# Kernel tuning notes

Measured on AMD Instinct MI355X. Metric: run time of the kernel, lower is better.

## Reference

```python
import jax, jax.numpy as jnp
import numpy as np

B, L, H, NH = 4, 2048, 1024, 8
DK = H // NH   # head_k_dim = 128
DV = H // NH   # head_v_dim = 128
CONV_K, FIR_S, FIR_L = 4, 3, 31
CMAX = 0.2
EPS = 1e-5
CHUNK = 32


def _l2norm(x):
    return x * jax.lax.rsqrt(jnp.sum(x * x, -1, keepdims=True) + 1e-6)


def _rms(x, w):
    return x * jax.lax.rsqrt(jnp.mean(x * x, -1, keepdims=True) + EPS) * w


def _causal_conv(x, w):
    # x: [b, l, d], w: [d, K] depthwise causal FIR (ShortConvolution)
    K = w.shape[1]
    l = x.shape[1]
    xp = jnp.pad(x, ((0, 0), (K - 1, 0), (0, 0)))
    return sum(xp[:, i:i + l, :] * w[:, i][None, None, :] for i in range(K))


def _fir(x, w):
    # x: [b, l, h, d], w: [h, d, K] per-head depthwise causal FIR
    K = w.shape[-1]
    l = x.shape[1]
    xp = jnp.pad(x, ((0, 0), (K - 1, 0), (0, 0), (0, 0)))
    return sum(xp[:, i:i + l] * w[:, :, i][None, None] for i in range(K))


def _delta_rule_chunkwise(q, k, v, beta, chunk=CHUNK):
    # q,k: [b,h,L,dk]; v: [b,h,L,dv]; beta: [b,h,L]; L % chunk == 0
    b, h, Ln, dk = q.shape
    dv = v.shape[-1]
    n = Ln // chunk
    q = _l2norm(q)
    k = _l2norm(k)
    v = v * beta[..., None]
    kb = k * beta[..., None]
    rs = lambda t: t.reshape(b, h, n, chunk, t.shape[-1])
    qc, kc, vc, kbc = rs(q), rs(k), rs(v), rs(kb)
    mask_incl = jnp.triu(jnp.ones((chunk, chunk), dtype=bool), 0)
    mask_strict = jnp.triu(jnp.ones((chunk, chunk), dtype=bool), 1)
    # UT / WY transform: sequential Gaussian-elimination over chunk rows
    attn = jnp.where(mask_incl, 0.0, -(kbc @ jnp.swapaxes(kc, -1, -2)))
    for i in range(1, chunk):
        row = attn[..., i, :]                                   # [b,h,n,c]
        upd = jnp.einsum('bhnj,bhnjk->bhnk', row, attn[..., :i])  # [b,h,n,i]
        attn = attn.at[..., i, :i].add(upd)
    attn = attn + jnp.eye(chunk, dtype=attn.dtype)
    u = attn @ vc    # [b,h,n,c,dv]
    w = attn @ kbc   # [b,h,n,c,dk]
    # sequential scan over chunks carrying state S [b,h,dk,dv]
    mv = lambda t: jnp.moveaxis(t, 2, 0)  # [n,b,h,c,d]
    def step(S, xs):
        q_i, k_i, u_i, w_i = xs
        attn_local = jnp.where(mask_strict, 0.0, q_i @ jnp.swapaxes(k_i, -1, -2))
        u_new = u_i - w_i @ S
        o_i = q_i @ S + attn_local @ u_new
        S = S + jnp.swapaxes(k_i, -1, -2) @ u_new
        return S, o_i
    S0 = jnp.zeros((b, h, dk, dv), dtype=q.dtype)
    S, o = jax.lax.scan(step, S0, (mv(qc), mv(kc), mv(u), mv(w)))
    o = jnp.moveaxis(o, 0, 2).reshape(b, h, Ln, dv)
    return o, S


def _forward(hidden_states, Wq, Wk, Wv, Wb, conv_q_w, conv_k_w, conv_v_w,
             fir_short_w, fir_long_w, floor_W, floor_b, fus_W1, fus_b1,
             fus_W2, fus_b2, norm_pf_w, norm_o_w, Wo):
    b, l, _ = hidden_states.shape
    hs = hidden_states
    q_lin = jax.nn.silu(_causal_conv(hs @ Wq, conv_q_w))
    k_lin = jax.nn.silu(_causal_conv(hs @ Wk, conv_k_w))
    v_lin = jax.nn.silu(_causal_conv(hs @ Wv, conv_v_w))
    q = q_lin.reshape(b, l, NH, DK)
    k = k_lin.reshape(b, l, NH, DK)
    v_direct = v_lin.reshape(b, l, NH, DV)
    beta = jax.nn.sigmoid(hs @ Wb)  # [b,l,h]
    delta_out_t, _ = _delta_rule_chunkwise(
        jnp.transpose(q, (0, 2, 1, 3)), jnp.transpose(k, (0, 2, 1, 3)),
        jnp.transpose(v_direct, (0, 2, 1, 3)), jnp.transpose(beta, (0, 2, 1)))
    delta_out = jnp.transpose(delta_out_t, (0, 2, 1, 3))  # [b,l,h,dv]
    local_short = _fir(v_direct, fir_short_w)
    local_long = _fir(v_direct, fir_long_w)
    floor = jax.nn.sigmoid(hs @ floor_W + floor_b) * CMAX  # [b,l,h]
    fus = jax.nn.gelu(hs @ fus_W1 + fus_b1, approximate=False) @ fus_W2 + fus_b2
    fus = fus.reshape(b, l, NH, 4)
    p_value = jax.nn.sigmoid(fus[..., 3]) * (1.0 - floor)  # context share >= floor
    ctx = jax.nn.softmax(fus[..., :3], axis=-1) * (1.0 - p_value)[..., None]
    o = (ctx[..., 0, None] * local_short + ctx[..., 1, None] * local_long
         + ctx[..., 2, None] * delta_out + p_value[..., None] * v_direct)
    o = _rms(o, norm_pf_w)
    o = _rms(o, norm_o_w)
    return o.reshape(b, l, NH * DV) @ Wo


def setup_inputs() -> dict:
    key = jax.random.key(0)
    ks = jax.random.split(key, 16)
    n = lambda k, shape, s=0.02: jax.random.normal(k, shape, jnp.float32) * s
    fus_b2 = jnp.zeros((NH * 4,), jnp.float32).at[3::4].set(4.0)
    return {
        'hidden_states': jax.random.normal(ks[0], (B, L, H), jnp.float32),
        'Wq': n(ks[1], (H, H)), 'Wk': n(ks[2], (H, H)), 'Wv': n(ks[3], (H, H)),
        'Wb': n(ks[4], (H, NH)),
        'conv_q_w': n(ks[5], (H, CONV_K), 0.2),
        'conv_k_w': n(ks[6], (H, CONV_K), 0.2),
        'conv_v_w': n(ks[7], (H, CONV_K), 0.2),
        'fir_short_w': n(ks[8], (NH, DV, FIR_S), 0.2),
        'fir_long_w': n(ks[9], (NH, DV, FIR_L), 0.2),
        'floor_W': n(ks[10], (H, NH)),
        'floor_b': jnp.full((NH,), float(np.log(CMAX / (1 - CMAX))), jnp.float32),
        'fus_W1': n(ks[11], (H, 2 * H)), 'fus_b1': jnp.zeros((2 * H,), jnp.float32),
        'fus_W2': n(ks[12], (2 * H, NH * 4)), 'fus_b2': fus_b2,
        'norm_pf_w': jnp.ones((DV,), jnp.float32),
        'norm_o_w': jnp.ones((DV,), jnp.float32),
        'Wo': n(ks[13], (H, H)),
    }


def reference(hidden_states, Wq, Wk, Wv, Wb, conv_q_w, conv_k_w, conv_v_w,
              fir_short_w, fir_long_w, floor_W, floor_b, fus_W1, fus_b1,
              fus_W2, fus_b2, norm_pf_w, norm_o_w, Wo):
    return _forward(hidden_states, Wq, Wk, Wv, Wb, conv_q_w, conv_k_w, conv_v_w,
                    fir_short_w, fir_long_w, floor_W, floor_b, fus_W1, fus_b1,
                    fus_W2, fus_b2, norm_pf_w, norm_o_w, Wo)
```

## Files before the change

kernel.cpp:

```cpp
#include <hip/hip_runtime.h>
#include <hip/hip_bf16.h>
#include <cstdint>
#include <cstddef>

#define DEVI static __device__ __forceinline__

typedef __attribute__((ext_vector_type(4))) float f32x4;
typedef __attribute__((ext_vector_type(8))) short s16x8;
typedef unsigned short u16;
typedef unsigned int u32;

DEVI float bf2f(u16 u){ u32 x = ((u32)u) << 16; float f; __builtin_memcpy(&f, &x, 4); return f; }
DEVI u16 f2bf(float f){ u32 x; __builtin_memcpy(&x, &f, 4); u32 r = x + 0x7fffu + ((x >> 16) & 1u); return (u16)(r >> 16); }
DEVI float sigm(float x){ return 1.0f / (1.0f + expf(-x)); }
DEVI f32x4 mfma16(s16x8 a, s16x8 b, f32x4 c){ return __builtin_amdgcn_mfma_f32_16x16x32_bf16(a, b, c, 0, 0, 0); }
DEVI s16x8 pack8(float4 a, float4 b){
  s16x8 v;
  v[0]=(short)f2bf(a.x); v[1]=(short)f2bf(a.y); v[2]=(short)f2bf(a.z); v[3]=(short)f2bf(a.w);
  v[4]=(short)f2bf(b.x); v[5]=(short)f2bf(b.y); v[6]=(short)f2bf(b.z); v[7]=(short)f2bf(b.w);
  return v;
}
DEVI u32 pkbf(float lo, float hi){
  u32 d; asm("v_cvt_pk_bf16_f32 %0, %1, %2" : "=v"(d) : "v"(lo), "v"(hi));
  return d;
}
DEVI s16x8 ld_tr(const u16* p){
  short4 a = *(const short4*)p;
  short4 b = *(const short4*)(p + 4);
  s16x8 v; v[0]=a.x; v[1]=a.y; v[2]=a.z; v[3]=a.w; v[4]=b.x; v[5]=b.y; v[6]=b.z; v[7]=b.w;
  return v;
}

#define GLL16(gp, lp) __builtin_amdgcn_global_load_lds( \
    (const __attribute__((address_space(1))) void*)(gp), \
    (__attribute__((address_space(3))) void*)(lp), 16, 0, 0)

__global__ __launch_bounds__(256) void cvt_bf16_k(const float* __restrict__ src, u16* __restrict__ dst, int n4){
  int i = blockIdx.x * 256 + threadIdx.x;
  if (i < n4){
    float4 v = ((const float4*)src)[i];
    ushort4 o; o.x = f2bf(v.x); o.y = f2bf(v.y); o.z = f2bf(v.z); o.w = f2bf(v.w);
    ((ushort4*)dst)[i] = o;
  }
}

__global__ __launch_bounds__(256) void transpose_bf16_k(const float* __restrict__ src, u16* __restrict__ dst, int K, int N){
  __shared__ float tile[32][33];
  const int n0 = blockIdx.x * 32, k0 = blockIdx.y * 32;
  const int t = threadIdx.x, cc = t & 31, rb = t >> 5;
  #pragma unroll
  for (int it = 0; it < 4; ++it){ int rr = rb + it*8; tile[rr][cc] = src[(size_t)(k0+rr)*N + n0 + cc]; }
  __syncthreads();
  #pragma unroll
  for (int it = 0; it < 4; ++it){ int rr = rb + it*8; dst[(size_t)(n0+rr)*K + k0 + cc] = f2bf(tile[cc][rr]); }
}

__global__ __launch_bounds__(64) void w2pack_k(const float* __restrict__ W2, u16* __restrict__ w2p){
  const int kt = blockIdx.x, nt = blockIdx.y;
  const int lane = threadIdx.x, g = lane >> 4, r = lane & 15;
  float v[8];
  #pragma unroll
  for (int i=0;i<8;++i) v[i] = W2[(size_t)(kt*32 + g*8 + i)*32 + nt*16 + r];
  *(s16x8*)(w2p + (((size_t)kt*2 + nt)*64 + lane)*8) = pack8(make_float4(v[0],v[1],v[2],v[3]),
                                                             make_float4(v[4],v[5],v[6],v[7]));
}

__global__ __launch_bounds__(64) void wbpack_k(const float* __restrict__ Wb, const float* __restrict__ Wfl,
                                              u16* __restrict__ wbp){
  const int kt = blockIdx.x;
  const int lane = threadIdx.x, g = lane >> 4, r = lane & 15;
  float v[8];
  #pragma unroll
  for (int i=0;i<8;++i){
    const int k = kt*32 + g*8 + i;
    v[i] = (r < 8) ? Wb[(size_t)k*8 + r] : Wfl[(size_t)k*8 + (r-8)];
  }
  *(s16x8*)(wbp + ((size_t)kt*64 + lane)*8) = pack8(make_float4(v[0],v[1],v[2],v[3]),
                                                    make_float4(v[4],v[5],v[6],v[7]));
}

template<int EPI>
__global__ __launch_bounds__(256, 2) void gemm_bt(
    const u16* __restrict__ A, const u16* __restrict__ Bt, void* __restrict__ Cout,
    const float* __restrict__ bias, int M, int N, int K)
{
  __shared__ __align__(16) u16 As[128*64];
  __shared__ __align__(16) u16 Bs[128*64];
  const int t = threadIdx.x;
  const int lane = t & 63, w = t >> 6;
  const int wr = w >> 1, wc = w & 1;
  const int g = lane >> 4, r16 = lane & 15;
  const int nwg = gridDim.x * gridDim.y;
  const int bid = blockIdx.x + blockIdx.y * gridDim.x;
  const int swz = (bid & 7) * (nwg >> 3) + (bid >> 3);
  const int m0 = (swz / gridDim.x) * 128, n0 = (swz % gridDim.x) * 128;
  f32x4 acc[4][4];
  #pragma unroll
  for (int i=0;i<4;++i){ f32x4 z = {0,0,0,0}; acc[i][0]=z; acc[i][1]=z; acc[i][2]=z; acc[i][3]=z; }
  const int NK = K / 64;
  const int slot_l = w*64 + lane;
  for (int kt = 0; kt < NK; ++kt){
    __syncthreads();
    #pragma unroll
    for (int j=0;j<4;++j){
      const int sl = j*256 + slot_l;
      const int row = sl >> 3, ch = sl & 7;
      const int chs = ch ^ (row & 7);
      GLL16(A  + (size_t)(m0+row)*K + kt*64 + chs*8, As + (size_t)(j*256 + w*64)*8);
      GLL16(Bt + (size_t)(n0+row)*K + kt*64 + chs*8, Bs + (size_t)(j*256 + w*64)*8);
    }
    __syncthreads();
    #pragma unroll
    for (int kh = 0; kh < 2; ++kh){
      s16x8 af[4], bf_[4];
      #pragma unroll
      for (int i=0;i<4;++i){
        const int arow = wr*64 + i*16 + r16;
        af[i]  = *(const s16x8*)(As + (size_t)arow*64 + (((4*kh+g) ^ (arow&7)))*8);
        const int brow = wc*64 + i*16 + r16;
        bf_[i] = *(const s16x8*)(Bs + (size_t)brow*64 + (((4*kh+g) ^ (brow&7)))*8);
      }
      #pragma unroll
      for (int mi=0;mi<4;++mi)
        #pragma unroll
        for (int ni=0;ni<4;++ni)
          acc[mi][ni] = mfma16(af[mi], bf_[ni], acc[mi][ni]);
    }
  }
  #pragma unroll
  for (int mi=0;mi<4;++mi)
    #pragma unroll
    for (int ni=0;ni<4;++ni){
      const int col = n0 + wc*64 + ni*16 + r16;
      #pragma unroll
      for (int i=0;i<4;++i){
        const int row = m0 + wr*64 + mi*16 + g*4 + i;
        float v = acc[mi][ni][i];
        if (EPI == 0){
          ((u16*)Cout)[(size_t)row*N + col] = f2bf(v);
        } else if (EPI == 1){
          float x = v + bias[col];
          x = 0.5f * x * (1.0f + erff(x * 0.70710678118f));
          ((u16*)Cout)[(size_t)row*N + col] = f2bf(x);
        } else if (EPI == 2){
          ((float*)Cout)[(size_t)row*N + col] = v;
        } else {
          ((u16*)Cout)[(size_t)(col >> 10)*8388608 + (size_t)row*1024 + (col & 1023)] = f2bf(v);
        }
      }
    }
}

__global__ __launch_bounds__(64) void beta_floor_k(
    const u16* __restrict__ hsb, const u16* __restrict__ wbp, const float* __restrict__ flb,
    float* __restrict__ beta, float* __restrict__ flo)
{
  const int m0 = blockIdx.x * 16;
  const int lane = threadIdx.x, g = lane >> 4, r = lane & 15;
  f32x4 acc0 = {0,0,0,0}, acc1 = {0,0,0,0};
  #pragma unroll 4
  for (int kt = 0; kt < 32; kt += 2){
    s16x8 a0 = *(const s16x8*)(hsb + (size_t)(m0+r)*1024 + kt*32 + g*8);
    s16x8 b0 = *(const s16x8*)(wbp + ((size_t)kt*64 + lane)*8);
    s16x8 a1 = *(const s16x8*)(hsb + (size_t)(m0+r)*1024 + (kt+1)*32 + g*8);
    s16x8 b1 = *(const s16x8*)(wbp + ((size_t)(kt+1)*64 + lane)*8);
    acc0 = mfma16(a0, b0, acc0);
    acc1 = mfma16(a1, b1, acc1);
  }
  const float fb = (r >= 8) ? flb[r-8] : 0.f;
  #pragma unroll
  for (int i=0;i<4;++i){
    const int row = m0 + g*4 + i;
    const float v = acc0[i] + acc1[i];
    if (r < 8) beta[(size_t)row*8 + r] = sigm(v);
    else       flo [(size_t)row*8 + (r-8)] = 0.2f * sigm(v + fb);
  }
}

__global__ __launch_bounds__(256) void conv_silu_k(
    const u16* __restrict__ qraw, const u16* __restrict__ kraw, const u16* __restrict__ vraw,
    const float* __restrict__ cwq, const float* __restrict__ cwk, const float* __restrict__ cwv,
    u16* __restrict__ vdir, u16* __restrict__ qn, u16* __restrict__ kn)
{
  const int blk = blockIdx.x;
  const int b = blk >> 7, lt = blk & 127;
  const int l0 = lt * 16;
  const int t = threadIdx.x, c0 = t * 4;
  float wq[16], wk[16], wv[16];
  #pragma unroll
  for (int cc=0; cc<4; ++cc){
    float4 a = *(const float4*)(cwq + (size_t)(c0+cc)*4);
    wq[cc*4+0]=a.x; wq[cc*4+1]=a.y; wq[cc*4+2]=a.z; wq[cc*4+3]=a.w;
    float4 bq = *(const float4*)(cwk + (size_t)(c0+cc)*4);
    wk[cc*4+0]=bq.x; wk[cc*4+1]=bq.y; wk[cc*4+2]=bq.z; wk[cc*4+3]=bq.w;
    float4 c = *(const float4*)(cwv + (size_t)(c0+cc)*4);
    wv[cc*4+0]=c.x; wv[cc*4+1]=c.y; wv[cc*4+2]=c.z; wv[cc*4+3]=c.w;
  }
  float hq[3][4], hk[3][4], hv[3][4];
  #pragma unroll
  for (int i=0;i<3;++i){
    const int ls = l0 - 3 + i;
    if (ls >= 0){
      const size_t base = ((size_t)(b << 11) + ls)*1024 + c0;
      union{ ushort4 v; u16 s[4]; } xq, xk, xv;
      xq.v = *(const ushort4*)(qraw + base);
      xk.v = *(const ushort4*)(kraw + base);
      xv.v = *(const ushort4*)(vraw + base);
      #pragma unroll
      for (int cc=0;cc<4;++cc){ hq[i][cc]=bf2f(xq.s[cc]); hk[i][cc]=bf2f(xk.s[cc]); hv[i][cc]=bf2f(xv.s[cc]); }
    } else {
      #pragma unroll
      for (int cc=0;cc<4;++cc){ hq[i][cc]=0.f; hk[i][cc]=0.f; hv[i][cc]=0.f; }
    }
  }
  float cq[4], ck4[4], cv4[4], nq[4], nk[4], nv[4];
  {
    const size_t base = ((size_t)(b << 11) + l0)*1024 + c0;
    union{ ushort4 v; u16 s[4]; } xq, xk, xv;
    xq.v = *(const ushort4*)(qraw + base);
    xk.v = *(const ushort4*)(kraw + base);
    xv.v = *(const ushort4*)(vraw + base);
    #pragma unroll
    for (int cc=0;cc<4;++cc){ cq[cc]=bf2f(xq.s[cc]); ck4[cc]=bf2f(xk.s[cc]); cv4[cc]=bf2f(xv.s[cc]); }
  }
  const int head = c0 >> 7, d0 = c0 & 127;
  for (int rr = 0; rr < 16; ++rr){
    const int l = l0 + rr;
    if (rr < 15){
      const size_t base = ((size_t)(b << 11) + l + 1)*1024 + c0;
      union{ ushort4 v; u16 s[4]; } xq, xk, xv;
      xq.v = *(const ushort4*)(qraw + base);
      xk.v = *(const ushort4*)(kraw + base);
      xv.v = *(const ushort4*)(vraw + base);
      #pragma unroll
      for (int cc=0;cc<4;++cc){ nq[cc]=bf2f(xq.s[cc]); nk[cc]=bf2f(xk.s[cc]); nv[cc]=bf2f(xv.s[cc]); }
    }
    float qa[4], ka[4], va[4];
    #pragma unroll
    for (int cc=0; cc<4; ++cc){
      qa[cc] = hq[0][cc]*wq[cc*4+0] + hq[1][cc]*wq[cc*4+1] + hq[2][cc]*wq[cc*4+2] + cq[cc]*wq[cc*4+3];
      ka[cc] = hk[0][cc]*wk[cc*4+0] + hk[1][cc]*wk[cc*4+1] + hk[2][cc]*wk[cc*4+2] + ck4[cc]*wk[cc*4+3];
      va[cc] = hv[0][cc]*wv[cc*4+0] + hv[1][cc]*wv[cc*4+1] + hv[2][cc]*wv[cc*4+2] + cv4[cc]*wv[cc*4+3];
    }
    #pragma unroll
    for (int cc=0; cc<4; ++cc){
      qa[cc] = qa[cc]*sigm(qa[cc]); ka[cc] = ka[cc]*sigm(ka[cc]); va[cc] = va[cc]*sigm(va[cc]);
    }
    const int grow = (b << 11) + l;
    ushort4 ov; ov.x=f2bf(va[0]); ov.y=f2bf(va[1]); ov.z=f2bf(va[2]); ov.w=f2bf(va[3]);
    *(ushort4*)(vdir + (size_t)grow*1024 + c0) = ov;
    float ssq = 0.f, ssk = 0.f;
    #pragma unroll
    for (int cc=0; cc<4; ++cc){ ssq += qa[cc]*qa[cc]; ssk += ka[cc]*ka[cc]; }
    #pragma unroll
    for (int m=1; m<32; m<<=1){ ssq += __shfl_xor(ssq, m, 64); ssk += __shfl_xor(ssk, m, 64); }
    const float rq = rsqrtf(ssq + 1e-6f), rk = rsqrtf(ssk + 1e-6f);
    const size_t ob = (((size_t)(b*8 + head))*2048 + l)*128 + d0;
    ushort4 oq, ok;
    oq.x=f2bf(qa[0]*rq); oq.y=f2bf(qa[1]*rq); oq.z=f2bf(qa[2]*rq); oq.w=f2bf(qa[3]*rq);
    ok.x=f2bf(ka[0]*rk); ok.y=f2bf(ka[1]*rk); ok.z=f2bf(ka[2]*rk); ok.w=f2bf(ka[3]*rk);
    *(ushort4*)(qn + ob) = oq;
    *(ushort4*)(kn + ob) = ok;
    #pragma unroll
    for (int cc=0; cc<4; ++cc){
      hq[0][cc]=hq[1][cc]; hq[1][cc]=hq[2][cc]; hq[2][cc]=cq[cc];  cq[cc]=nq[cc];
      hk[0][cc]=hk[1][cc]; hk[1][cc]=hk[2][cc]; hk[2][cc]=ck4[cc]; ck4[cc]=nk[cc];
      hv[0][cc]=hv[1][cc]; hv[1][cc]=hv[2][cc]; hv[2][cc]=cv4[cc]; cv4[cc]=nv[cc];
    }
  }
}

__global__ __launch_bounds__(64) void fus2_k(
    const u16* __restrict__ A, const u16* __restrict__ w2p, const float* __restrict__ b2,
    float* __restrict__ out)
{
  const int m0 = blockIdx.x * 16;
  const int lane = threadIdx.x, g = lane >> 4, r = lane & 15;
  f32x4 acc[2][2];
  #pragma unroll
  for (int nt=0;nt<2;++nt){ f32x4 z = {0,0,0,0}; acc[nt][0]=z; acc[nt][1]=z; }
  #pragma unroll 4
  for (int kt = 0; kt < 64; ++kt){
    s16x8 af = *(const s16x8*)(A + (size_t)(m0+r)*2048 + kt*32 + g*8);
    s16x8 b0 = *(const s16x8*)(w2p + (((size_t)kt*2 + 0)*64 + lane)*8);
    s16x8 b1 = *(const s16x8*)(w2p + (((size_t)kt*2 + 1)*64 + lane)*8);
    acc[0][kt&1] = mfma16(af, b0, acc[0][kt&1]);
    acc[1][kt&1] = mfma16(af, b1, acc[1][kt&1]);
  }
  #pragma unroll
  for (int nt=0;nt<2;++nt){
    const float bb = b2[nt*16 + r];
    #pragma unroll
    for (int i=0;i<4;++i)
      out[(size_t)(m0 + g*4 + i)*32 + nt*16 + r] = acc[nt][0][i] + acc[nt][1][i] + bb;
  }
}

__global__ __launch_bounds__(256, 2) void ut_k(
    const u16* __restrict__ qn, const u16* __restrict__ kn,
    const u16* __restrict__ vdir, const float* __restrict__ beta,
    u16* __restrict__ alocp, u16* __restrict__ updk,
    u16* __restrict__ wpk, u16* __restrict__ knpk)
{
  __shared__ __align__(16) char smem[39680];
  u16*  k_s = (u16*)smem;
  float* Tm = (float*)smem;
  float* Gm = (float*)(smem + 8192);
  float* al = (float*)(smem + 12416);
  float* wl = (float*)(smem + 8192);
  u16*  knT = (u16*)(smem + 17024);
  u16*  vbT = (u16*)(smem + 28288);
  float* bet = (float*)(smem + 39552);

  const int blk = blockIdx.x;
  const int ic = blk & 63, bh = blk >> 6;
  const int b = bh >> 3, h = bh & 7;
  const int l0 = ic * 32;
  const int t = threadIdx.x;
  const int lane = t & 63, w = t >> 6;
  const int g = lane >> 4, r = lane & 15;
  const int mt = w >> 1, nt_g = w & 1;

  const size_t gqk = ((size_t)bh*2048 + l0)*128;

  {
    const int row = t >> 3, sseg = t & 7;
    #pragma unroll
    for (int ss=0; ss<2; ++ss){
      const int s = sseg + ss*8;
      int4 kv = *(const int4*)(kn + gqk + (size_t)row*128 + s*8);
      *(int4*)((char*)k_s + row*256 + ((s ^ (row&7))*16)) = kv;
    }
  }
  {
    const int rp = t & 15, cs = t >> 4;
    const int r0 = 2*rp, r1 = 2*rp + 1;
    union { s16x8 v; u16 u[8]; } k0, k1, v0, v1;
    k0.v = *(const s16x8*)(kn + gqk + (size_t)r0*128 + cs*8);
    k1.v = *(const s16x8*)(kn + gqk + (size_t)r1*128 + cs*8);
    v0.v = *(const s16x8*)(vdir + ((size_t)b*2048 + l0 + r0)*1024 + h*128 + cs*8);
    v1.v = *(const s16x8*)(vdir + ((size_t)b*2048 + l0 + r1)*1024 + h*128 + cs*8);
    const float be0 = beta[((size_t)b*2048 + l0 + r0)*8 + h];
    const float be1 = beta[((size_t)b*2048 + l0 + r1)*8 + h];
    if (t < 32) bet[t] = beta[((size_t)b*2048 + l0 + t)*8 + h];
    #pragma unroll
    for (int i=0;i<8;++i){
      const int d = cs*8 + i;
      *(u32*)(knT + (size_t)d*44 + r0) = (u32)k0.u[i] | ((u32)k1.u[i] << 16);
      u32 lo = f2bf(bf2f(v0.u[i]) * be0);
      u32 hi = f2bf(bf2f(v1.u[i]) * be1);
      *(u32*)(vbT + (size_t)d*44 + r0) = lo | (hi << 16);
    }
  }
  __syncthreads();

  {
    f32x4 gacc = {0,0,0,0}, aacc = {0,0,0,0};
    #pragma unroll
    for (int kt=0; kt<4; ++kt){
      s16x8 afk = *(const s16x8*)(kn + gqk + (size_t)(mt*16+r)*128 + kt*32 + g*8);
      s16x8 afq = *(const s16x8*)(qn + gqk + (size_t)(mt*16+r)*128 + kt*32 + g*8);
      const int brow = nt_g*16 + r;
      s16x8 bfrag = *(const s16x8*)((const char*)k_s + brow*256 + (((kt*4+g) ^ (brow&7))*16));
      gacc = mfma16(afk, bfrag, gacc);
      aacc = mfma16(afq, bfrag, aacc);
    }
    #pragma unroll
    for (int i=0;i<4;++i){
      const int rr = mt*16 + g*4 + i, cc = nt_g*16 + r;
      Gm[rr*33 + cc] = gacc[i];
      al[rr*36 + cc] = (cc <= rr) ? aacc[i] : 0.f;
    }
  }
  __syncthreads();

  if (w == 0){
    const int kk = lane & 15, grp = (lane >> 4) & 1, b0 = grp*16;
    float tc[16];
    #pragma unroll
    for (int j=0;j<16;++j)
      tc[j] = (j > kk) ? (-bet[b0+j] * Gm[(b0+j)*33 + b0+kk]) : 0.f;
    #pragma unroll
    for (int i=1;i<16;++i){
      float upd = 0.f;
      #pragma unroll
      for (int j=0;j<i;++j) upd += __shfl(tc[i], (lane & 48) + j, 64) * tc[j];
      if (kk < i) tc[i] += upd;
    }
    if (lane < 32){
      #pragma unroll
      for (int j=0;j<16;++j) Tm[(b0+j)*36 + b0+kk] = tc[j] + ((j == kk) ? 1.f : 0.f);
      if (grp == 1){
        #pragma unroll
        for (int j=0;j<16;++j) Tm[j*36 + 16 + kk] = 0.f;
      }
    }
  } else if (w == 1){
    #pragma unroll
    for (int m2=0; m2<2; ++m2){
      float4 z0 = *(const float4*)(al + (m2*16+r)*36 + g*8);
      float4 z1 = *(const float4*)(al + (m2*16+r)*36 + g*8 + 4);
      *(s16x8*)(alocp + (((size_t)blk*2 + m2)*64 + lane)*8) = pack8(z0, z1);
    }
  } else {
    #pragma unroll
    for (int q2=0; q2<4; ++q2){
      const int mtd = (w-2)*4 + q2;
      s16x8 vv = ld_tr(knT + (size_t)(mtd*16+r)*44 + g*8);
      *(s16x8*)(knpk + (((size_t)blk*8 + mtd)*64 + lane)*8) = vv;
    }
  }
  __syncthreads();

  {
    const int kP = t >> 4, cP = t & 15;
    float p = 0.f;
    #pragma unroll
    for (int m=0;m<16;++m) p += Gm[(16+kP)*33 + m] * Tm[m*36 + cP];
    al[kP*36 + cP] = -bet[16+kP] * p;
  }
  __syncthreads();

  {
    const int rT = t >> 4, cT = t & 15;
    float s = 0.f;
    #pragma unroll
    for (int k=0;k<16;++k) s += Tm[(16+rT)*36 + 16 + k] * al[k*36 + cT];
    Tm[(16+rT)*36 + cT] = s;
  }
  __syncthreads();

  {
    float bb[8];
    #pragma unroll
    for (int i=0;i<8;++i) bb[i] = bet[g*8+i];
    s16x8 tA[2];
    #pragma unroll
    for (int m2=0; m2<2; ++m2){
      float4 x0 = *(const float4*)(Tm + (m2*16+r)*36 + g*8);
      float4 x1 = *(const float4*)(Tm + (m2*16+r)*36 + g*8 + 4);
      tA[m2] = pack8(x0, x1);
    }
    #pragma unroll
    for (int rr2=0; rr2<2; ++rr2){
      const int nt = rr2*4 + w;
      s16x8 bu   = ld_tr(vbT + (size_t)(nt*16+r)*44 + g*8);
      s16x8 braw = ld_tr(knT + (size_t)(nt*16+r)*44 + g*8);
      s16x8 bw;
      #pragma unroll
      for (int i=0;i<8;++i) bw[i] = (short)f2bf(bf2f((u16)braw[i]) * bb[i]);
      f32x4 zz = {0,0,0,0};
      f32x4 du0 = mfma16(tA[0], bu, zz);
      f32x4 du1 = mfma16(tA[1], bu, zz);
      f32x4 dw0 = mfma16(tA[0], bw, zz);
      f32x4 dw1 = mfma16(tA[1], bw, zz);
      *(s16x8*)(updk + (((size_t)blk*8 + nt)*64 + lane)*8) =
          pack8(make_float4(du0[0],du0[1],du0[2],du0[3]),
                make_float4(du1[0],du1[1],du1[2],du1[3]));
      #pragma unroll
      for (int i=0;i<4;++i){
        wl[(      g*4 + i)*68 + (nt&3)*16 + r] = -dw0[i];
        wl[(16 +  g*4 + i)*68 + (nt&3)*16 + r] = -dw1[i];
      }
      __syncthreads();
      {
        const int mtp = w >> 1, ktp = rr2*2 + (w & 1);
        float4 y0 = *(const float4*)(wl + (mtp*16+r)*68 + (ktp&1)*32 + g*8);
        float4 y1 = *(const float4*)(wl + (mtp*16+r)*68 + (ktp&1)*32 + g*8 + 4);
        *(s16x8*)(wpk + ((((size_t)blk*2 + mtp)*4 + ktp)*64 + lane)*8) = pack8(y0, y1);
      }
      __syncthreads();
    }
  }
}

struct SBuf {
  s16x8 uraw;
  s16x8 wf[8];
  s16x8 q0[4], q1[4];
  s16x8 a0, a1;
  s16x8 kf[8];
};

DEVI void scan_load(SBuf& b, const u16* up, const u16* wp, const u16* qp,
                    const u16* ap, const u16* kp, int r, int g){
  b.uraw = *(const s16x8*)(up);
  #pragma unroll
  for (int j=0;j<8;++j) b.wf[j] = *(const s16x8*)(wp + j*512);
  #pragma unroll
  for (int kt=0;kt<4;++kt){
    b.q0[kt] = *(const s16x8*)(qp + r*128 + kt*32 + g*8);
    b.q1[kt] = *(const s16x8*)(qp + (16+r)*128 + kt*32 + g*8);
  }
  b.a0 = *(const s16x8*)(ap);
  b.a1 = *(const s16x8*)(ap + 512);
  #pragma unroll
  for (int j=0;j<8;++j) b.kf[j] = *(const s16x8*)(kp + j*512);
}

DEVI void scan_step(const SBuf& b, f32x4* Sf, u16* dptr,
                    int srcA, int srcB, bool hi, int r, int g){
  u32 pk0[8], pk1[8];
  #pragma unroll
  for (int m=0;m<8;++m){
    pk0[m] = pkbf(Sf[m][0], Sf[m][1]);
    pk1[m] = pkbf(Sf[m][2], Sf[m][3]);
  }
  s16x8 sf[4];
  #pragma unroll
  for (int kt=0;kt<4;++kt){
    u32 eA0 = __shfl(pk0[kt*2],   srcA, 64), oA0 = __shfl(pk0[kt*2+1], srcA, 64);
    u32 eA1 = __shfl(pk1[kt*2],   srcA, 64), oA1 = __shfl(pk1[kt*2+1], srcA, 64);
    u32 eB0 = __shfl(pk0[kt*2],   srcB, 64), oB0 = __shfl(pk0[kt*2+1], srcB, 64);
    u32 eB1 = __shfl(pk1[kt*2],   srcB, 64), oB1 = __shfl(pk1[kt*2+1], srcB, 64);
    union { u32 w[4]; s16x8 v; } uw;
    uw.w[0] = hi ? oA0 : eA0;
    uw.w[1] = hi ? oA1 : eA1;
    uw.w[2] = hi ? oB0 : eB0;
    uw.w[3] = hi ? oB1 : eB1;
    sf[kt] = uw.v;
  }
  f32x4 unA, unB, unA2 = {0,0,0,0}, unB2 = {0,0,0,0};
  #pragma unroll
  for (int i=0;i<4;++i){ unA[i] = bf2f((u16)b.uraw[i]); unB[i] = bf2f((u16)b.uraw[4+i]); }
  unA  = mfma16(b.wf[0], sf[0], unA);
  unA2 = mfma16(b.wf[2], sf[2], unA2);
  unB  = mfma16(b.wf[4], sf[0], unB);
  unB2 = mfma16(b.wf[6], sf[2], unB2);
  unA  = mfma16(b.wf[1], sf[1], unA);
  unA2 = mfma16(b.wf[3], sf[3], unA2);
  unB  = mfma16(b.wf[5], sf[1], unB);
  unB2 = mfma16(b.wf[7], sf[3], unB2);
  f32x4 o0 = {0,0,0,0}, o1 = {0,0,0,0};
  #pragma unroll
  for (int kt=0;kt<4;++kt){
    o0 = mfma16(b.q0[kt], sf[kt], o0);
    o1 = mfma16(b.q1[kt], sf[kt], o1);
  }
  unA = unA + unA2;
  unB = unB + unB2;
  u32 a0p0 = pkbf(unA[0], unA[1]), a0p1 = pkbf(unA[2], unA[3]);
  u32 a1p0 = pkbf(unB[0], unB[1]), a1p1 = pkbf(unB[2], unB[3]);
  u32 w00 = __shfl(a0p0, srcA, 64), w10 = __shfl(a1p0, srcA, 64);
  u32 w01 = __shfl(a0p1, srcA, 64), w11 = __shfl(a1p1, srcA, 64);
  u32 w02 = __shfl(a0p0, srcB, 64), w12 = __shfl(a1p0, srcB, 64);
  u32 w03 = __shfl(a0p1, srcB, 64), w13 = __shfl(a1p1, srcB, 64);
  union { u32 w[4]; s16x8 v; } uu;
  uu.w[0] = hi ? w10 : w00;
  uu.w[1] = hi ? w11 : w01;
  uu.w[2] = hi ? w12 : w02;
  uu.w[3] = hi ? w13 : w03;
  const s16x8 uf = uu.v;
  o0 = mfma16(b.a0, uf, o0);
  o1 = mfma16(b.a1, uf, o1);
  #pragma unroll
  for (int i=0;i<4;++i){
    dptr[(size_t)(g*4+i)*128]    = f2bf(o0[i]);
    dptr[(size_t)(16+g*4+i)*128] = f2bf(o1[i]);
  }
  #pragma unroll
  for (int m=0;m<8;++m) Sf[m] = mfma16(b.kf[m], uf, Sf[m]);
}

__global__ __launch_bounds__(64, 1) void scan_k(
    const u16* __restrict__ qn, const u16* __restrict__ wpk,
    const u16* __restrict__ updk, const u16* __restrict__ alocp,
    const u16* __restrict__ knpk, u16* __restrict__ delta)
{
  const int blk = blockIdx.x;
  const int sl = blk >> 5, bh = blk & 31;
  const int lane = threadIdx.x;
  const int g = lane >> 4, r = lane & 15;
  const int srcA = (g & 1)*32 + r;
  const int srcB = srcA + 16;
  const bool hi = (g >= 2);
  f32x4 Sf[8];
  #pragma unroll
  for (int m=0;m<8;++m){ f32x4 z = {0,0,0,0}; Sf[m] = z; }

  const u16* upB = updk + ((size_t)bh*64*8 + sl)*512 + (size_t)lane*8;
  const u16* wpB = wpk  + (size_t)bh*64*4096 + (size_t)lane*8;
  const u16* qpB = qn   + (size_t)bh*2048*128;
  const u16* apB = alocp + (size_t)bh*64*1024 + (size_t)lane*8;
  const u16* kpB = knpk + (size_t)bh*64*4096 + (size_t)lane*8;
  u16*       dB  = delta + (size_t)bh*2048*128 + sl*16 + r;

  SBuf A, B;
  scan_load(A, upB, wpB, qpB, apB, kpB, r, g);
  for (int ic = 0; ic < 64; ic += 2){
    scan_load(B, upB + (size_t)(ic+1)*4096, wpB + (size_t)(ic+1)*4096,
              qpB + (size_t)(ic+1)*4096, apB + (size_t)(ic+1)*1024,
              kpB + (size_t)(ic+1)*4096, r, g);
    scan_step(A, Sf, dB + (size_t)ic*4096, srcA, srcB, hi, r, g);
    if (ic + 2 < 64)
      scan_load(A, upB + (size_t)(ic+2)*4096, wpB + (size_t)(ic+2)*4096,
                qpB + (size_t)(ic+2)*4096, apB + (size_t)(ic+2)*1024,
                kpB + (size_t)(ic+2)*4096, r, g);
    scan_step(B, Sf, dB + (size_t)(ic+1)*4096, srcA, srcB, hi, r, g);
  }
}

__global__ __launch_bounds__(256) void fuse_k(
    const u16* __restrict__ vdir, const u16* __restrict__ delta,
    const float* __restrict__ fusv, const float* __restrict__ flo,
    const float* __restrict__ fsw, const float* __restrict__ flw,
    const float* __restrict__ wpf, const float* __restrict__ wno,
    u16* __restrict__ ofin)
{
  __shared__ float fl_t[31][128];
  const int blk = blockIdx.x;
  const int lt = blk & 31, h = (blk >> 5) & 7, b = blk >> 8;
  const int t = threadIdx.x;
  const int w = t >> 6, lane = t & 63;
  const int d0 = lane * 2;
  const int l0 = lt*64 + w*16;
  for (int j = t; j < 3968; j += 256){
    const int d = j / 31, i = j - d*31;
    fl_t[i][d] = flw[(size_t)h*3968 + j];
  }
  __syncthreads();
  float wlo[46], whi[46];
  #pragma unroll
  for (int j = 0; j < 46; ++j){
    const int ls = l0 - 30 + j;
    u32 x = 0;
    if (ls >= 0) x = *(const u32*)(vdir + ((size_t)b*2048 + ls)*1024 + h*128 + d0);
    wlo[j] = bf2f((u16)(x & 0xffffu));
    whi[j] = bf2f((u16)(x >> 16));
  }
  float lg0[16], lg1[16];
  #pragma unroll
  for (int rr = 0; rr < 16; ++rr){ lg0[rr] = 0.f; lg1[rr] = 0.f; }
  #pragma unroll
  for (int i = 0; i < 31; ++i){
    const float2 wv = *(const float2*)&fl_t[i][d0];
    #pragma unroll
    for (int rr = 0; rr < 16; ++rr){
      lg0[rr] += wlo[rr + i] * wv.x;
      lg1[rr] += whi[rr + i] * wv.y;
    }
  }
  const float wp0 = wpf[d0], wp1 = wpf[d0+1];
  const float wn0 = wno[d0], wn1 = wno[d0+1];
  float fs0[3], fs1[3];
  #pragma unroll
  for (int i=0;i<3;++i){
    fs0[i] = fsw[((size_t)h*128 + d0)*3 + i];
    fs1[i] = fsw[((size_t)h*128 + d0 + 1)*3 + i];
  }
  #pragma unroll
  for (int rr = 0; rr < 16; ++rr){
    const int l = l0 + rr;
    const float* fr = fusv + ((size_t)b*2048 + l)*32 + h*4;
    const float f0=fr[0], f1=fr[1], f2=fr[2], f3=fr[3];
    const float flv = flo[((size_t)b*2048 + l)*8 + h];
    const float p = sigm(f3) * (1.f - flv);
    const float mx = fmaxf(f0, fmaxf(f1, f2));
    const float e0 = expf(f0-mx), e1 = expf(f1-mx), e2 = expf(f2-mx);
    const float inv = (1.f - p) / (e0 + e1 + e2);
    const float c0 = e0*inv, c1 = e1*inv, c2 = e2*inv;
    const float sh0 = wlo[rr+28]*fs0[0] + wlo[rr+29]*fs0[1] + wlo[rr+30]*fs0[2];
    const float sh1 = whi[rr+28]*fs1[0] + whi[rr+29]*fs1[1] + whi[rr+30]*fs1[2];
    const u32 dl2 = *(const u32*)(delta + (((size_t)(b*8 + h))*2048 + l)*128 + d0);
    const float dlx = bf2f((u16)(dl2 & 0xffffu)), dly = bf2f((u16)(dl2 >> 16));
    float o0 = c0*sh0 + c1*lg0[rr] + c2*dlx + p*wlo[rr+30];
    float o1 = c0*sh1 + c1*lg1[rr] + c2*dly + p*whi[rr+30];
    const float b0 = o0*wp0, b1 = o1*wp1;
    float ss = o0*o0 + o1*o1;
    float tt = b0*b0 + b1*b1;
    #pragma unroll
    for (int m=1; m<64; m<<=1){
      ss += __shfl_xor(ss, m, 64);
      tt += __shfl_xor(tt, m, 64);
    }
    const float r1 = rsqrtf(ss * (1.f/128.f) + 1e-5f);
    const float r2 = rsqrtf(r1*r1*tt * (1.f/128.f) + 1e-5f);
    const u32 h0 = f2bf(o0*r1*wp0*r2*wn0), h1 = f2bf(o1*r1*wp1*r2*wn1);
    *(u32*)(ofin + ((size_t)b*2048 + l)*1024 + h*128 + d0) = h0 | (h1 << 16);
  }
}

constexpr size_t OFF_HSB  = 0;
constexpr size_t OFF_WQT  = 16777216;
constexpr size_t OFF_WKT  = 18874368;
constexpr size_t OFF_WVT  = 20971520;
constexpr size_t OFF_W1T  = 23068672;
constexpr size_t OFF_WOT  = 27262976;
constexpr size_t OFF_QRAW = 29360128;
constexpr size_t OFF_KRAW = 46137344;
constexpr size_t OFF_VRAW = 62914560;
constexpr size_t OFF_FUSV = 79691776;
constexpr size_t OFF_BETA = 80740352;
constexpr size_t OFF_FLO  = 81002496;
constexpr size_t OFF_VDIR = 81264640;
constexpr size_t OFF_W2P  = 98041856;
constexpr size_t OFF_WBP  = 98172928;
constexpr size_t OFF_QN   = 114819072;
constexpr size_t OFF_KN   = 131596288;
constexpr size_t OFF_ALOC = 148373504;
constexpr size_t OFF_UPDK = 152567808;
constexpr size_t OFF_KNPK = 186122240;

extern "C" void kernel_launch(void* const* d_in, const int* in_sizes, int n_in,
                              void* d_out, int out_size, void* d_ws, size_t ws_size,
                              hipStream_t stream)
{
  const float* hs   = (const float*)d_in[0];
  const float* Wq   = (const float*)d_in[1];
  const float* Wk   = (const float*)d_in[2];
  const float* Wv   = (const float*)d_in[3];
  const float* Wb   = (const float*)d_in[4];
  const float* cq   = (const float*)d_in[5];
  const float* ck   = (const float*)d_in[6];
  const float* cv   = (const float*)d_in[7];
  const float* firs = (const float*)d_in[8];
  const float* firl = (const float*)d_in[9];
  const float* flW  = (const float*)d_in[10];
  const float* flb  = (const float*)d_in[11];
  const float* W1   = (const float*)d_in[12];
  const float* b1   = (const float*)d_in[13];
  const float* W2   = (const float*)d_in[14];
  const float* b2   = (const float*)d_in[15];
  const float* npf  = (const float*)d_in[16];
  const float* now  = (const float*)d_in[17];
  const float* Wo   = (const float*)d_in[18];

  char* ws = (char*)d_ws;
  u16*   hsb   = (u16*)(ws + OFF_HSB);
  u16*   wqT   = (u16*)(ws + OFF_WQT);
  u16*   wkT   = (u16*)(ws + OFF_WKT);
  u16*   wvT   = (u16*)(ws + OFF_WVT);
  u16*   w1T   = (u16*)(ws + OFF_W1T);
  u16*   woT   = (u16*)(ws + OFF_WOT);
  u16*   qraw  = (u16*)(ws + OFF_QRAW);
  u16*   kraw  = (u16*)(ws + OFF_KRAW);
  u16*   vraw  = (u16*)(ws + OFF_VRAW);
  u16*   fus1g = (u16*)(ws + OFF_QRAW);
  float* fusv  = (float*)(ws + OFF_FUSV);
  float* beta  = (float*)(ws + OFF_BETA);
  float* flo   = (float*)(ws + OFF_FLO);
  u16*   vdir  = (u16*)(ws + OFF_VDIR);
  u16*   w2p   = (u16*)(ws + OFF_W2P);
  u16*   wbp   = (u16*)(ws + OFF_WBP);
  u16*   qn    = (u16*)(ws + OFF_QN);
  u16*   kn    = (u16*)(ws + OFF_KN);
  u16*   alocp = (u16*)(ws + OFF_ALOC);
  u16*   updk  = (u16*)(ws + OFF_UPDK);
  u16*   wpk   = (u16*)(ws + OFF_VRAW);
  u16*   knpk  = (u16*)(ws + OFF_KNPK);
  u16*   delta = (u16*)(ws + OFF_QRAW);
  u16*   ofin  = (u16*)(ws + OFF_UPDK);

  cvt_bf16_k<<<8192, 256, 0, stream>>>(hs, hsb, 2097152);
  w2pack_k<<<dim3(64,2), 64, 0, stream>>>(W2, w2p);
  wbpack_k<<<32, 64, 0, stream>>>(Wb, flW, wbp);
  transpose_bf16_k<<<dim3(32,32), 256, 0, stream>>>(Wq, wqT, 1024, 1024);
  transpose_bf16_k<<<dim3(32,32), 256, 0, stream>>>(Wk, wkT, 1024, 1024);
  transpose_bf16_k<<<dim3(32,32), 256, 0, stream>>>(Wv, wvT, 1024, 1024);
  transpose_bf16_k<<<dim3(64,32), 256, 0, stream>>>(W1, w1T, 1024, 2048);
  transpose_bf16_k<<<dim3(32,32), 256, 0, stream>>>(Wo, woT, 1024, 1024);
  beta_floor_k<<<512, 64, 0, stream>>>(hsb, wbp, flb, beta, flo);
  gemm_bt<3><<<dim3(24,64), 256, 0, stream>>>(hsb, wqT, qraw, nullptr, 8192, 3072, 1024);
  conv_silu_k<<<512, 256, 0, stream>>>(qraw, kraw, vraw, cq, ck, cv, vdir, qn, kn);
  gemm_bt<1><<<dim3(16,64), 256, 0, stream>>>(hsb, w1T, fus1g, b1, 8192, 2048, 1024);
  fus2_k<<<512, 64, 0, stream>>>(fus1g, w2p, b2, fusv);
  ut_k<<<2048, 256, 0, stream>>>(qn, kn, vdir, beta, alocp, updk, wpk, knpk);
  scan_k<<<256, 64, 0, stream>>>(qn, wpk, updk, alocp, knpk, delta);
  fuse_k<<<1024, 256, 0, stream>>>(vdir, delta, fusv, flo, firs, firl, npf, now, ofin);
  gemm_bt<2><<<dim3(8,64), 256, 0, stream>>>(ofin, woT, d_out, nullptr, 8192, 1024, 1024);
}
```

Before: 350.2 us.

## Fuse QKV and fusion-MLP GEMMs, dual-chain scan per wave, fast exp

Merges the QKV projection and the first fusion-MLP GEMM into one 5120-wide GEMM with a split epilogue (bf16 scatter for QKV, bias+GELU for the MLP part). It relies on the transposed W1 sitting right after the QKV weights in the workspace. The scan kernel now handles two independent 16-column state slices per wave, sharing the w/q/k fragment loads, and launches half as many blocks. expf is swapped for __expf in sigmoid and softmax. These changes cut launches and redundant loads and add ILP to the latency-bound scan, at the cost of more registers and reduced exp precision.

```diff
diff --git a/kernel.cpp b/kernel.cpp
--- a/kernel.cpp
+++ b/kernel.cpp
@@ -12,7 +12,7 @@
 
 DEVI float bf2f(u16 u){ u32 x = ((u32)u) << 16; float f; __builtin_memcpy(&f, &x, 4); return f; }
 DEVI u16 f2bf(float f){ u32 x; __builtin_memcpy(&x, &f, 4); u32 r = x + 0x7fffu + ((x >> 16) & 1u); return (u16)(r >> 16); }
-DEVI float sigm(float x){ return 1.0f / (1.0f + expf(-x)); }
+DEVI float sigm(float x){ return 1.0f / (1.0f + __expf(-x)); }
 DEVI f32x4 mfma16(s16x8 a, s16x8 b, f32x4 c){ return __builtin_amdgcn_mfma_f32_16x16x32_bf16(a, b, c, 0, 0, 0); }
 DEVI s16x8 pack8(float4 a, float4 b){
   s16x8 v;
@@ -82,7 +82,7 @@
 template<int EPI>
 __global__ __launch_bounds__(256, 2) void gemm_bt(
     const u16* __restrict__ A, const u16* __restrict__ Bt, void* __restrict__ Cout,
-    const float* __restrict__ bias, int M, int N, int K)
+    void* __restrict__ Cout2, const float* __restrict__ bias, int M, int N, int K)
 {
   __shared__ __align__(16) u16 As[128*64];
   __shared__ __align__(16) u16 Bs[128*64];
@@ -144,8 +144,16 @@
           ((u16*)Cout)[(size_t)row*N + col] = f2bf(x);
         } else if (EPI == 2){
           ((float*)Cout)[(size_t)row*N + col] = v;
+        } else if (EPI == 3){
+          ((u16*)Cout)[(size_t)(col >> 10)*8388608 + (size_t)row*1024 + (col & 1023)] = f2bf(v);
         } else {
-          ((u16*)Cout)[(size_t)(col >> 10)*8388608 + (size_t)row*1024 + (col & 1023)] = f2bf(v);
+          if (col < 3072){
+            ((u16*)Cout)[(size_t)(col >> 10)*8388608 + (size_t)row*1024 + (col & 1023)] = f2bf(v);
+          } else {
+            float x = v + bias[col - 3072];
+            x = 0.5f * x * (1.0f + erff(x * 0.70710678118f));
+            ((u16*)Cout2)[(size_t)row*2048 + (col - 3072)] = f2bf(x);
+          }
         }
       }
     }
@@ -474,17 +482,16 @@
   }
 }
 
-struct SBuf {
-  s16x8 uraw;
+struct SShared {
   s16x8 wf[8];
   s16x8 q0[4], q1[4];
   s16x8 a0, a1;
   s16x8 kf[8];
 };
-
-DEVI void scan_load(SBuf& b, const u16* up, const u16* wp, const u16* qp,
-                    const u16* ap, const u16* kp, int r, int g){
-  b.uraw = *(const s16x8*)(up);
+struct SU { s16x8 u0, u1; };
+
+DEVI void load_sh(SShared& b, const u16* wp, const u16* qp, const u16* ap,
+                  const u16* kp, int r, int g){
   #pragma unroll
   for (int j=0;j<8;++j) b.wf[j] = *(const s16x8*)(wp + j*512);
   #pragma unroll
@@ -497,9 +504,13 @@
   #pragma unroll
   for (int j=0;j<8;++j) b.kf[j] = *(const s16x8*)(kp + j*512);
 }
-
-DEVI void scan_step(const SBuf& b, f32x4* Sf, u16* dptr,
-                    int srcA, int srcB, bool hi, int r, int g){
+DEVI void load_u(SU& u, const u16* up){
+  u.u0 = *(const s16x8*)(up);
+  u.u1 = *(const s16x8*)(up + 2048);
+}
+
+DEVI void scan_chain(const SShared& b, const s16x8 uraw, f32x4* Sf, u16* dptr,
+                     int srcA, int srcB, bool hi, int r, int g){
   u32 pk0[8], pk1[8];
   #pragma unroll
   for (int m=0;m<8;++m){
@@ -522,7 +533,7 @@
   }
   f32x4 unA, unB, unA2 = {0,0,0,0}, unB2 = {0,0,0,0};
   #pragma unroll
-  for (int i=0;i<4;++i){ unA[i] = bf2f((u16)b.uraw[i]); unB[i] = bf2f((u16)b.uraw[4+i]); }
+  for (int i=0;i<4;++i){ unA[i] = bf2f((u16)uraw[i]); unB[i] = bf2f((u16)uraw[4+i]); }
   unA  = mfma16(b.wf[0], sf[0], unA);
   unA2 = mfma16(b.wf[2], sf[2], unA2);
   unB  = mfma16(b.wf[4], sf[0], unB);
@@ -562,41 +573,52 @@
   for (int m=0;m<8;++m) Sf[m] = mfma16(b.kf[m], uf, Sf[m]);
 }
 
+DEVI void scan_step2(const SShared& sh, const SU& su, f32x4* Sf0, f32x4* Sf1,
+                     u16* d0, u16* d1, int srcA, int srcB, bool hi, int r, int g){
+  scan_chain(sh, su.u0, Sf0, d0, srcA, srcB, hi, r, g);
+  scan_chain(sh, su.u1, Sf1, d1, srcA, srcB, hi, r, g);
+}
+
 __global__ __launch_bounds__(64, 1) void scan_k(
     const u16* __restrict__ qn, const u16* __restrict__ wpk,
     const u16* __restrict__ updk, const u16* __restrict__ alocp,
     const u16* __restrict__ knpk, u16* __restrict__ delta)
 {
   const int blk = blockIdx.x;
-  const int sl = blk >> 5, bh = blk & 31;
+  const int sl0 = blk >> 5, bh = blk & 31;
   const int lane = threadIdx.x;
   const int g = lane >> 4, r = lane & 15;
   const int srcA = (g & 1)*32 + r;
   const int srcB = srcA + 16;
   const bool hi = (g >= 2);
-  f32x4 Sf[8];
-  #pragma unroll
-  for (int m=0;m<8;++m){ f32x4 z = {0,0,0,0}; Sf[m] = z; }
-
-  const u16* upB = updk + ((size_t)bh*64*8 + sl)*512 + (size_t)lane*8;
+  f32x4 Sf0[8], Sf1[8];
+  #pragma unroll
+  for (int m=0;m<8;++m){ f32x4 z = {0,0,0,0}; Sf0[m] = z; Sf1[m] = z; }
+
+  const u16* upB = updk + ((size_t)bh*64*8 + sl0)*512 + (size_t)lane*8;
   const u16* wpB = wpk  + (size_t)bh*64*4096 + (size_t)lane*8;
   const u16* qpB = qn   + (size_t)bh*2048*128;
   const u16* apB = alocp + (size_t)bh*64*1024 + (size_t)lane*8;
   const u16* kpB = knpk + (size_t)bh*64*4096 + (size_t)lane*8;
-  u16*       dB  = delta + (size_t)bh*2048*128 + sl*16 + r;
-
-  SBuf A, B;
-  scan_load(A, upB, wpB, qpB, apB, kpB, r, g);
+  u16*       dB0 = delta + (size_t)bh*2048*128 + sl0*16 + r;
+  u16*       dB1 = dB0 + 64;
+
+  SShared shA, shB; SU suA, suB;
+  load_sh(shA, wpB, qpB, apB, kpB, r, g);
+  load_u(suA, upB);
   for (int ic = 0; ic < 64; ic += 2){
-    scan_load(B, upB + (size_t)(ic+1)*4096, wpB + (size_t)(ic+1)*4096,
-              qpB + (size_t)(ic+1)*4096, apB + (size_t)(ic+1)*1024,
-              kpB + (size_t)(ic+1)*4096, r, g);
-    scan_step(A, Sf, dB + (size_t)ic*4096, srcA, srcB, hi, r, g);
-    if (ic + 2 < 64)
-      scan_load(A, upB + (size_t)(ic+2)*4096, wpB + (size_t)(ic+2)*4096,
-                qpB + (size_t)(ic+2)*4096, apB + (size_t)(ic+2)*1024,
-                kpB + (size_t)(ic+2)*4096, r, g);
-    scan_step(B, Sf, dB + (size_t)(ic+1)*4096, srcA, srcB, hi, r, g);
+    load_sh(shB, wpB + (size_t)(ic+1)*4096, qpB + (size_t)(ic+1)*4096,
+            apB + (size_t)(ic+1)*1024, kpB + (size_t)(ic+1)*4096, r, g);
+    load_u(suB, upB + (size_t)(ic+1)*4096);
+    scan_step2(shA, suA, Sf0, Sf1, dB0 + (size_t)ic*4096, dB1 + (size_t)ic*4096,
+               srcA, srcB, hi, r, g);
+    if (ic + 2 < 64){
+      load_sh(shA, wpB + (size_t)(ic+2)*4096, qpB + (size_t)(ic+2)*4096,
+              apB + (size_t)(ic+2)*1024, kpB + (size_t)(ic+2)*4096, r, g);
+      load_u(suA, upB + (size_t)(ic+2)*4096);
+    }
+    scan_step2(shB, suB, Sf0, Sf1, dB0 + (size_t)(ic+1)*4096, dB1 + (size_t)(ic+1)*4096,
+               srcA, srcB, hi, r, g);
   }
 }
 
@@ -656,7 +678,7 @@
     const float flv = flo[((size_t)b*2048 + l)*8 + h];
     const float p = sigm(f3) * (1.f - flv);
     const float mx = fmaxf(f0, fmaxf(f1, f2));
-    const float e0 = expf(f0-mx), e1 = expf(f1-mx), e2 = expf(f2-mx);
+    const float e0 = __expf(f0-mx), e1 = __expf(f1-mx), e2 = __expf(f2-mx);
     const float inv = (1.f - p) / (e0 + e1 + e2);
     const float c0 = e0*inv, c1 = e1*inv, c2 = e2*inv;
     const float sh0 = wlo[rr+28]*fs0[0] + wlo[rr+29]*fs0[1] + wlo[rr+30]*fs0[2];
@@ -735,7 +757,7 @@
   u16*   qraw  = (u16*)(ws + OFF_QRAW);
   u16*   kraw  = (u16*)(ws + OFF_KRAW);
   u16*   vraw  = (u16*)(ws + OFF_VRAW);
-  u16*   fus1g = (u16*)(ws + OFF_QRAW);
+  u16*   fus1g = (u16*)(ws + OFF_UPDK);
   float* fusv  = (float*)(ws + OFF_FUSV);
   float* beta  = (float*)(ws + OFF_BETA);
   float* flo   = (float*)(ws + OFF_FLO);
@@ -760,12 +782,11 @@
   transpose_bf16_k<<<dim3(64,32), 256, 0, stream>>>(W1, w1T, 1024, 2048);
   transpose_bf16_k<<<dim3(32,32), 256, 0, stream>>>(Wo, woT, 1024, 1024);
   beta_floor_k<<<512, 64, 0, stream>>>(hsb, wbp, flb, beta, flo);
-  gemm_bt<3><<<dim3(24,64), 256, 0, stream>>>(hsb, wqT, qraw, nullptr, 8192, 3072, 1024);
+  gemm_bt<4><<<dim3(40,64), 256, 0, stream>>>(hsb, wqT, qraw, fus1g, b1, 8192, 5120, 1024);
+  fus2_k<<<512, 64, 0, stream>>>(fus1g, w2p, b2, fusv);
   conv_silu_k<<<512, 256, 0, stream>>>(qraw, kraw, vraw, cq, ck, cv, vdir, qn, kn);
-  gemm_bt<1><<<dim3(16,64), 256, 0, stream>>>(hsb, w1T, fus1g, b1, 8192, 2048, 1024);
-  fus2_k<<<512, 64, 0, stream>>>(fus1g, w2p, b2, fusv);
   ut_k<<<2048, 256, 0, stream>>>(qn, kn, vdir, beta, alocp, updk, wpk, knpk);
-  scan_k<<<256, 64, 0, stream>>>(qn, wpk, updk, alocp, knpk, delta);
+  scan_k<<<128, 64, 0, stream>>>(qn, wpk, updk, alocp, knpk, delta);
   fuse_k<<<1024, 256, 0, stream>>>(vdir, delta, fusv, flo, firs, firl, npf, now, ofin);
-  gemm_bt<2><<<dim3(8,64), 256, 0, stream>>>(ofin, woT, d_out, nullptr, 8192, 1024, 1024);
-}
+  gemm_bt<2><<<dim3(8,64), 256, 0, stream>>>(ofin, woT, d_out, nullptr, nullptr, 8192, 1024, 1024);
+}
```

Measured after the change: 413.4 us. 18.0% more time.
